# Optimization experiments

Measured on AMD Instinct MI355X. Metric: run time of the kernel, lower is better.

Reference implementation:

```python
import jax, jax.numpy as jnp
import numpy as np

NUM_HEADS = 4
HEAD_DIM = 128  # out_dim // num_heads = 512 // 4
TOP_K = 16
NEG_SLOPE = 0.2


def setup_inputs() -> dict:
    key = jax.random.key(0)
    k1, k2, k3, k4 = jax.random.split(key, 4)
    N, in_dim, out_dim = 4096, 1024, 512
    x = jax.random.normal(k1, (N, in_dim), dtype=jnp.float32)
    adj = jax.random.uniform(k2, (N, N), dtype=jnp.float32)  # all-positive, like softmax attn
    W = jax.random.normal(k3, (out_dim, in_dim), dtype=jnp.float32) * 0.02
    a = jax.random.normal(k4, (1, 2 * HEAD_DIM), dtype=jnp.float32) * 0.02
    return {"x": x, "adj": adj, "W": W, "a": a}


def reference(x, adj, W, a):
    N = x.shape[0]
    Wh = (x @ W.T).reshape(N, NUM_HEADS, HEAD_DIM)  # (N, H, D)

    # _sparsify_adj: keep top-k per row, binary mask
    k = min(TOP_K, N)
    _, topk_idx = jax.lax.top_k(adj, k)  # (N, k)
    rows = jnp.arange(N)[:, None]
    sparse = jnp.zeros_like(adj).at[rows, topk_idx].set(1.0)
    mask = sparse > 0  # (N_i, N_j)

    # a([Wh_i, Wh_j]) decomposed: a = [a_src | a_dst], score = s_i + s_j
    a_src, a_dst = a[0, :HEAD_DIM], a[0, HEAD_DIM:]
    s_i = jnp.einsum("nhd,d->nh", Wh, a_src)  # (N, H)
    s_j = jnp.einsum("nhd,d->nh", Wh, a_dst)  # (N, H)
    e = jax.nn.leaky_relu(s_i[:, None, :] + s_j[None, :, :], NEG_SLOPE)  # (N_i, N_j, H)
    e = jnp.where(mask[:, :, None], e, -jnp.inf)

    alpha = jax.nn.softmax(e, axis=1)  # softmax over neighbors j
    alpha = jnp.nan_to_num(alpha, nan=0.0)

    out = jnp.einsum("imh,mhd->ihd", alpha, Wh)  # weighted sum over j
    return jax.nn.elu(out.reshape(N, -1))  # (N, out_dim)
```

## Files before the change

### kernel.cpp

```cpp
#include <hip/hip_runtime.h>
#include <hip/hip_bf16.h>

#define N_NODES 4096
#define IN_DIM 1024
#define OUT_DIM 512
#define NUM_HEADS 4
#define HEAD_DIM 128
#define TOP_K 16
#define NEG_SLOPE 0.2f

typedef __attribute__((ext_vector_type(8))) short bf16x8;
typedef __attribute__((ext_vector_type(4))) float f32x4;

typedef __attribute__((address_space(3))) unsigned as3_u32;
typedef const __attribute__((address_space(1))) unsigned as1_u32;

static __device__ __forceinline__ void gld16(const void* g, void* l) {
    __builtin_amdgcn_global_load_lds((as1_u32*)g, (as3_u32*)l, 16, 0, 0);
}

__device__ __forceinline__ unsigned short f2bf(float f) {
    unsigned u = __float_as_uint(f);
    unsigned r = u + 0x7FFFu + ((u >> 16) & 1u);
    return (unsigned short)(r >> 16);
}
__device__ __forceinline__ float bf2f(unsigned short h) {
    return __uint_as_float(((unsigned)h) << 16);
}

__device__ __forceinline__ void conv_row(const float* __restrict__ src,
                                         unsigned short* __restrict__ dst, int t)
{
    int row = t >> 7, rem = t & 127, kb = rem >> 2, c = rem & 3;
    const float* s = src + (size_t)row * IN_DIM + kb * 32 + c * 8;
    float4 v0 = *(const float4*)s;
    float4 v1 = *(const float4*)(s + 4);
    float vv[8] = {v0.x, v0.y, v0.z, v0.w, v1.x, v1.y, v1.z, v1.w};
    bf16x8 H, L;
#pragma unroll
    for (int e = 0; e < 8; ++e) {
        unsigned short h = f2bf(vv[e]);
        H[e] = (short)h;
        L[e] = (short)f2bf(vv[e] - bf2f(h));
    }
    int sw = row & 7;
    unsigned short* base = dst + (size_t)row * 2048 + kb * 64;
    *(bf16x8*)(base + ((c ^ sw) << 3))       = H;
    *(bf16x8*)(base + (((c + 4) ^ sw) << 3)) = L;
}

#define TK_THRESH 0.988f

__device__ __forceinline__ void topk_body(int row, const float* __restrict__ adj,
                                          int* __restrict__ topkb)
{
    const int tid  = threadIdx.x;
    const int wave = tid >> 6, lane = tid & 63;
    const float* rp = adj + (size_t)row * N_NODES;

    __shared__ unsigned long long cand[4][64];
    __shared__ int wcnt[4];
    __shared__ float srow[N_NODES];

    float4 q0 = *(const float4*)(rp + wave * 1024 + 0 * 256 + lane * 4);
    float4 q1 = *(const float4*)(rp + wave * 1024 + 1 * 256 + lane * 4);
    float4 q2 = *(const float4*)(rp + wave * 1024 + 2 * 256 + lane * 4);
    float4 q3 = *(const float4*)(rp + wave * 1024 + 3 * 256 + lane * 4);

    const unsigned long long lmask = (1ull << lane) - 1ull;
    int cnt = 0;

#define FILT(qv, i, e, comp) do {                                             \
        float val = (qv).comp;                                                \
        int g = wave * 1024 + (i) * 256 + lane * 4 + (e);                     \
        bool p = val >= TK_THRESH;                                            \
        unsigned long long m = __ballot(p);                                   \
        if (p) {                                                              \
            int pos = cnt + __popcll(m & lmask);                              \
            if (pos < 64) {                                                   \
                unsigned b  = __float_as_uint(val);                           \
                unsigned mo = b ^ (unsigned)(((int)b >> 31) | 0x80000000);    \
                cand[wave][pos] =                                             \
                    ((unsigned long long)mo << 32) | (unsigned)(N_NODES - 1 - g); \
            }                                                                 \
        }                                                                     \
        cnt += __popcll(m);                                                   \
    } while (0)

    FILT(q0, 0, 0, x); FILT(q0, 0, 1, y); FILT(q0, 0, 2, z); FILT(q0, 0, 3, w);
    FILT(q1, 1, 0, x); FILT(q1, 1, 1, y); FILT(q1, 1, 2, z); FILT(q1, 1, 3, w);
    FILT(q2, 2, 0, x); FILT(q2, 2, 1, y); FILT(q2, 2, 2, z); FILT(q2, 2, 3, w);
    FILT(q3, 3, 0, x); FILT(q3, 3, 1, y); FILT(q3, 3, 2, z); FILT(q3, 3, 3, w);
#undef FILT

    if (lane == 0) wcnt[wave] = cnt;
    __syncthreads();

    const int c0n = wcnt[0], c1n = wcnt[1], c2n = wcnt[2], c3n = wcnt[3];
    const int total = c0n + c1n + c2n + c3n;
    const bool ok = (total >= TOP_K) &&
                    (c0n <= 64) && (c1n <= 64) && (c2n <= 64) && (c3n <= 64);
    int* op = topkb + (size_t)row * TOP_K;

    if (ok) {
        if (wave == 0) {
            unsigned long long k0 = lane < c0n ? cand[0][lane] : 0ull;
            unsigned long long k1 = lane < c1n ? cand[1][lane] : 0ull;
            unsigned long long k2 = lane < c2n ? cand[2][lane] : 0ull;
            unsigned long long k3 = lane < c3n ? cand[3][lane] : 0ull;
            for (int r = 0; r < TOP_K; ++r) {
                unsigned long long a01 = k0 > k1 ? k0 : k1;
                unsigned long long a23 = k2 > k3 ? k2 : k3;
                unsigned long long b = a01 > a23 ? a01 : a23;
#pragma unroll
                for (int m = 1; m < 64; m <<= 1) {
                    unsigned long long o = __shfl_xor(b, m);
                    b = o > b ? o : b;
                }
                if (lane == 0) op[r] = N_NODES - 1 - (int)(unsigned)(b & 0xFFFFFFFFu);
                if (k0 == b) k0 = 0ull;
                if (k1 == b) k1 = 0ull;
                if (k2 == b) k2 = 0ull;
                if (k3 == b) k3 = 0ull;
            }
        }
    } else {
        int base = wave * 1024 + lane * 4;
        *(float4*)&srow[base + 0 * 256] = q0;
        *(float4*)&srow[base + 1 * 256] = q1;
        *(float4*)&srow[base + 2 * 256] = q2;
        *(float4*)&srow[base + 3 * 256] = q3;
        __syncthreads();
        if (wave == 0) {
            for (int r = 0; r < TOP_K; ++r) {
                float bv = -INFINITY; int bg = 0x7fffffff;
                for (int j = 0; j < 64; ++j) {
                    int g = j * 64 + lane;
                    float val = srow[g];
                    bool better = (val > bv) || (val == bv && g < bg);
                    bv = better ? val : bv;
                    bg = better ? g : bg;
                }
#pragma unroll
                for (int m = 1; m < 64; m <<= 1) {
                    float ov = __shfl_xor(bv, m);
                    int   og = __shfl_xor(bg, m);
                    bool better = (ov > bv) || (ov == bv && og < bg);
                    bv = better ? ov : bv;
                    bg = better ? og : bg;
                }
                if (lane == 0) { op[r] = bg; srow[bg] = -INFINITY; }
            }
        }
    }
}

__global__ __launch_bounds__(256) void prep_topk_kernel(
    const float* __restrict__ x, const float* __restrict__ W,
    unsigned short* __restrict__ xc, unsigned short* __restrict__ wc,
    const float* __restrict__ adj, int* __restrict__ topkb)
{
    int b = blockIdx.x, tid = threadIdx.x;
    if (b < 4096) {
        topk_body(b, adj, topkb);
    } else if (b < 6144) {
        conv_row(x, xc, (b - 4096) * 256 + tid);
    } else {
        conv_row(W, wc, (b - 6144) * 256 + tid);
    }
}

#define GBM 64
#define GBN 64

__global__ __launch_bounds__(256, 2) void gemm_kernel(
    const unsigned short* __restrict__ xc, const unsigned short* __restrict__ wc,
    const float* __restrict__ a, unsigned short* __restrict__ Whb,
    float* __restrict__ spart)
{
    __shared__ __align__(16) unsigned short A0[GBM * 64];
    __shared__ __align__(16) unsigned short A1[GBM * 64];
    __shared__ __align__(16) unsigned short A2[GBM * 64];
    __shared__ __align__(16) unsigned short A3[GBM * 64];
    __shared__ __align__(16) unsigned short B0[GBN * 64];
    __shared__ __align__(16) unsigned short B1[GBN * 64];
    __shared__ __align__(16) unsigned short B2[GBN * 64];
    __shared__ __align__(16) unsigned short B3[GBN * 64];

    const int tid = threadIdx.x;
    const int id  = blockIdx.x;
    const int xcd = id & 7, seq = id >> 3;
    const int bm  = xcd * 8 + (seq >> 3), bn = seq & 7;

    const int wave = tid >> 6, lane = tid & 63;
    const int wm = wave >> 1, wn = wave & 1;
    const int lr = lane & 15, lk = lane >> 4;

    f32x4 acc[2][2];
#pragma unroll
    for (int i = 0; i < 2; ++i)
#pragma unroll
        for (int j = 0; j < 2; ++j) acc[i][j] = (f32x4){0.f, 0.f, 0.f, 0.f};

#define STAGE(Abuf, Bbuf, kt) do {                                            \
        size_t koff = (size_t)(kt) * 128;                                     \
        _Pragma("unroll")                                                     \
        for (int q = 0; q < 2; ++q) {               \
            int ci = q * 256 + tid;                                           \
            int row = ci >> 3, p = ci & 7;                                    \
            gld16((const char*)xc + ((size_t)(bm * GBM + row) * 4096 + koff + p * 16), \
                  (char*)(Abuf) + (size_t)ci * 16);                           \
        }                                                                     \
        _Pragma("unroll")                                                     \
        for (int q = 0; q < 2; ++q) {               \
            int ci = q * 256 + tid;                                           \
            int row = ci >> 3, p = ci & 7;                                    \
            gld16((const char*)wc + ((size_t)(bn * GBN + row) * 4096 + koff + p * 16), \
                  (char*)(Bbuf) + (size_t)ci * 16);                           \
        }                                                                     \
    } while (0)

#define COMPUTE(Abuf, Bbuf) do {                                              \
        bf16x8 bh[2], bl[2];                                                  \
        _Pragma("unroll")                                                     \
        for (int ni = 0; ni < 2; ++ni) {                                      \
            int rb = wn * 32 + ni * 16 + lr; int swb = rb & 7;                \
            bh[ni] = *(const bf16x8*)&(Bbuf)[rb * 64 + ((lk ^ swb) << 3)];    \
            bl[ni] = *(const bf16x8*)&(Bbuf)[rb * 64 + (((4 + lk) ^ swb) << 3)]; \
        }                                                                     \
        __builtin_amdgcn_s_setprio(1);                                        \
        _Pragma("unroll")                                                     \
        for (int mi = 0; mi < 2; ++mi) {                                      \
            int r = wm * 32 + mi * 16 + lr; int sw = r & 7;                   \
            bf16x8 ah = *(const bf16x8*)&(Abuf)[r * 64 + ((lk ^ sw) << 3)];   \
            bf16x8 al = *(const bf16x8*)&(Abuf)[r * 64 + (((4 + lk) ^ sw) << 3)]; \
            _Pragma("unroll")                                                 \
            for (int ni = 0; ni < 2; ++ni) {                                  \
                acc[mi][ni] = __builtin_amdgcn_mfma_f32_16x16x32_bf16(ah, bh[ni], acc[mi][ni], 0, 0, 0); \
                acc[mi][ni] = __builtin_amdgcn_mfma_f32_16x16x32_bf16(ah, bl[ni], acc[mi][ni], 0, 0, 0); \
                acc[mi][ni] = __builtin_amdgcn_mfma_f32_16x16x32_bf16(al, bh[ni], acc[mi][ni], 0, 0, 0); \
            }                                                                 \
        }                                                                     \
        __builtin_amdgcn_s_setprio(0);                                        \
    } while (0)

#define BODY(Ac, Bc, An, Bn, ktn, W) do {                                     \
        asm volatile("s_waitcnt vmcnt(" #W ")" ::: "memory");                 \
        __builtin_amdgcn_s_barrier();                                         \
        asm volatile("" ::: "memory");                                        \
        if ((ktn) < 32) STAGE(An, Bn, ktn);                                   \
        COMPUTE(Ac, Bc);                                                      \
    } while (0)

    STAGE(A0, B0, 0);
    STAGE(A1, B1, 1);
    STAGE(A2, B2, 2);

    for (int i = 0; i < 7; ++i) {
        BODY(A0, B0, A3, B3, i * 4 + 3, 8);
        BODY(A1, B1, A0, B0, i * 4 + 4, 8);
        BODY(A2, B2, A1, B1, i * 4 + 5, 8);
        BODY(A3, B3, A2, B2, i * 4 + 6, 8);
    }
    BODY(A0, B0, A3, B3, 31, 8);
    BODY(A1, B1, A0, B0, 33, 8);
    asm volatile("s_waitcnt vmcnt(4)" ::: "memory");
    __builtin_amdgcn_s_barrier();
    asm volatile("" ::: "memory");
    COMPUTE(A2, B2);
    asm volatile("s_waitcnt vmcnt(0)" ::: "memory");
    __builtin_amdgcn_s_barrier();
    asm volatile("" ::: "memory");
    COMPUTE(A3, B3);

#undef BODY
#undef COMPUTE
#undef STAGE

    const int h = bn >> 1;
    float* sps = spart + ((size_t)((bn & 1) * 2 + wn)) * 16384;
    float* spd = spart + 65536 + ((size_t)((bn & 1) * 2 + wn)) * 16384;
    float ca[2], cb[2];
#pragma unroll
    for (int ni = 0; ni < 2; ++ni) {
        int dcol = (bn & 1) * 64 + wn * 32 + ni * 16 + lr;
        ca[ni] = a[dcol];
        cb[ni] = a[HEAD_DIM + dcol];
    }
#pragma unroll
    for (int mi = 0; mi < 2; ++mi) {
        float ss[4] = {0.f, 0.f, 0.f, 0.f}, sd[4] = {0.f, 0.f, 0.f, 0.f};
#pragma unroll
        for (int ni = 0; ni < 2; ++ni) {
            int col_g = bn * GBN + wn * 32 + ni * 16 + lr;
#pragma unroll
            for (int r = 0; r < 4; ++r) {
                int row_g = bm * GBM + wm * 32 + mi * 16 + lk * 4 + r;
                float v = acc[mi][ni][r];
                Whb[(size_t)row_g * OUT_DIM + col_g] = f2bf(v);
                ss[r] += v * ca[ni];
                sd[r] += v * cb[ni];
            }
        }
#pragma unroll
        for (int s = 1; s < 16; s <<= 1)
#pragma unroll
            for (int r = 0; r < 4; ++r) {
                ss[r] += __shfl_xor(ss[r], s);
                sd[r] += __shfl_xor(sd[r], s);
            }
        if (lr == 0) {
#pragma unroll
            for (int r = 0; r < 4; ++r) {
                int row_g = bm * GBM + wm * 32 + mi * 16 + lk * 4 + r;
                sps[row_g * NUM_HEADS + h] = ss[r];
                spd[row_g * NUM_HEADS + h] = sd[r];
            }
        }
    }
}

__global__ __launch_bounds__(256) void aggregate_kernel(
    const unsigned short* __restrict__ Whb, const int* __restrict__ topk,
    const float* __restrict__ spart, float* __restrict__ out)
{
    const int i = blockIdx.x, t = threadIdx.x;
    __shared__ int   sidx[TOP_K];
    __shared__ float salpha[TOP_K][NUM_HEADS];
    __shared__ float part[3][8][64];

    if (t < 64) {
        int idxv = 0;
        if (t < TOP_K) { idxv = topk[(size_t)i * TOP_K + t]; sidx[t] = idxv; }
        int m = t >> 2, h = t & 3;
        int im = __shfl(idxv, m);
        int si = (i << 2) + h, di = (im << 2) + h;
        float e = spart[si] + spart[16384 + si] + spart[32768 + si] + spart[49152 + si]
                + spart[65536 + di] + spart[81920 + di] + spart[98304 + di] + spart[114688 + di];
        e = (e >= 0.f) ? e : NEG_SLOPE * e;
        float mx = e;
#pragma unroll
        for (int s = 4; s < 64; s <<= 1) mx = fmaxf(mx, __shfl_xor(mx, s));
        float ex = expf(e - mx);
        float sum = ex;
#pragma unroll
        for (int s = 4; s < 64; s <<= 1) sum += __shfl_xor(sum, s);
        salpha[m][h] = ex / sum;
    }
    __syncthreads();

    const int g = t >> 6, o = t & 63;
    const int h = o >> 4;
    float acc8[8] = {0.f, 0.f, 0.f, 0.f, 0.f, 0.f, 0.f, 0.f};
#pragma unroll
    for (int q = 0; q < 4; ++q) {
        int m = g * 4 + q;
        float al = salpha[m][h];
        bf16x8 v = *(const bf16x8*)&Whb[(size_t)sidx[m] * OUT_DIM + o * 8];
#pragma unroll
        for (int e = 0; e < 8; ++e)
            acc8[e] += al * bf2f((unsigned short)v[e]);
    }
    if (g) {
#pragma unroll
        for (int e = 0; e < 8; ++e) part[g - 1][e][o] = acc8[e];
    }
    __syncthreads();
    if (!g) {
        float r8[8];
#pragma unroll
        for (int e = 0; e < 8; ++e) {
            float s = acc8[e] + part[0][e][o] + part[1][e][o] + part[2][e][o];
            r8[e] = s > 0.f ? s : expf(s) - 1.f;
        }
        float4 lo = (float4){r8[0], r8[1], r8[2], r8[3]};
        float4 hi = (float4){r8[4], r8[5], r8[6], r8[7]};
        *(float4*)(out + (size_t)i * OUT_DIM + o * 8)     = lo;
        *(float4*)(out + (size_t)i * OUT_DIM + o * 8 + 4) = hi;
    }
}

extern "C" void kernel_launch(void* const* d_in, const int* in_sizes, int n_in,
                              void* d_out, int out_size, void* d_ws, size_t ws_size,
                              hipStream_t stream) {
    const float* x   = (const float*)d_in[0];
    const float* adj = (const float*)d_in[1];
    const float* W   = (const float*)d_in[2];
    const float* a   = (const float*)d_in[3];
    float* out = (float*)d_out;

    char* ws = (char*)d_ws;
    unsigned short* Whb   = (unsigned short*)ws;
    unsigned short* xc    = (unsigned short*)(ws + (8u << 20));
    unsigned short* wc    = (unsigned short*)(ws + (24u << 20));
    float*          spart = (float*)(ws + (26u << 20));
    int*            topkb = (int*)(ws + (26u << 20) + (512u << 10));

    prep_topk_kernel<<<6400, 256, 0, stream>>>(x, W, xc, wc, adj, topkb);
    gemm_kernel<<<512, 256, 0, stream>>>(xc, wc, a, Whb, spart);
    aggregate_kernel<<<N_NODES, 256, 0, stream>>>(Whb, topkb, spart, out);
}
```

Measured before the change: 142.2 us.

## Fuse top-k selection into GEMM kernel as interleaved blocks

Moves the per-row top-k selection out of the conversion kernel into the GEMM launch, interleaving one GEMM block with eight top-k blocks (4608 blocks total). The memory-bound adjacency scan can then overlap the compute-bound MFMA GEMM instead of running in the earlier serial phase. Top-k blocks reuse the GEMM's LDS buffers for candidates and fallback row storage. The trade-off is that top-k blocks now inherit the GEMM's large LDS footprint and launch bounds, which can reduce how many of them are resident at once.

Result: slower. 195.0 us (+37.2%).

```diff
diff --git a/kernel.cpp b/kernel.cpp
--- a/kernel.cpp
+++ b/kernel.cpp
@@ -49,134 +49,24 @@
     *(bf16x8*)(base + (((c + 4) ^ sw) << 3)) = L;
 }
 
-#define TK_THRESH 0.988f
-
-__device__ __forceinline__ void topk_body(int row, const float* __restrict__ adj,
-                                          int* __restrict__ topkb)
-{
-    const int tid  = threadIdx.x;
-    const int wave = tid >> 6, lane = tid & 63;
-    const float* rp = adj + (size_t)row * N_NODES;
-
-    __shared__ unsigned long long cand[4][64];
-    __shared__ int wcnt[4];
-    __shared__ float srow[N_NODES];
-
-    float4 q0 = *(const float4*)(rp + wave * 1024 + 0 * 256 + lane * 4);
-    float4 q1 = *(const float4*)(rp + wave * 1024 + 1 * 256 + lane * 4);
-    float4 q2 = *(const float4*)(rp + wave * 1024 + 2 * 256 + lane * 4);
-    float4 q3 = *(const float4*)(rp + wave * 1024 + 3 * 256 + lane * 4);
-
-    const unsigned long long lmask = (1ull << lane) - 1ull;
-    int cnt = 0;
-
-#define FILT(qv, i, e, comp) do {                                             \
-        float val = (qv).comp;                                                \
-        int g = wave * 1024 + (i) * 256 + lane * 4 + (e);                     \
-        bool p = val >= TK_THRESH;                                            \
-        unsigned long long m = __ballot(p);                                   \
-        if (p) {                                                              \
-            int pos = cnt + __popcll(m & lmask);                              \
-            if (pos < 64) {                                                   \
-                unsigned b  = __float_as_uint(val);                           \
-                unsigned mo = b ^ (unsigned)(((int)b >> 31) | 0x80000000);    \
-                cand[wave][pos] =                                             \
-                    ((unsigned long long)mo << 32) | (unsigned)(N_NODES - 1 - g); \
-            }                                                                 \
-        }                                                                     \
-        cnt += __popcll(m);                                                   \
-    } while (0)
-
-    FILT(q0, 0, 0, x); FILT(q0, 0, 1, y); FILT(q0, 0, 2, z); FILT(q0, 0, 3, w);
-    FILT(q1, 1, 0, x); FILT(q1, 1, 1, y); FILT(q1, 1, 2, z); FILT(q1, 1, 3, w);
-    FILT(q2, 2, 0, x); FILT(q2, 2, 1, y); FILT(q2, 2, 2, z); FILT(q2, 2, 3, w);
-    FILT(q3, 3, 0, x); FILT(q3, 3, 1, y); FILT(q3, 3, 2, z); FILT(q3, 3, 3, w);
-#undef FILT
-
-    if (lane == 0) wcnt[wave] = cnt;
-    __syncthreads();
-
-    const int c0n = wcnt[0], c1n = wcnt[1], c2n = wcnt[2], c3n = wcnt[3];
-    const int total = c0n + c1n + c2n + c3n;
-    const bool ok = (total >= TOP_K) &&
-                    (c0n <= 64) && (c1n <= 64) && (c2n <= 64) && (c3n <= 64);
-    int* op = topkb + (size_t)row * TOP_K;
-
-    if (ok) {
-        if (wave == 0) {
-            unsigned long long k0 = lane < c0n ? cand[0][lane] : 0ull;
-            unsigned long long k1 = lane < c1n ? cand[1][lane] : 0ull;
-            unsigned long long k2 = lane < c2n ? cand[2][lane] : 0ull;
-            unsigned long long k3 = lane < c3n ? cand[3][lane] : 0ull;
-            for (int r = 0; r < TOP_K; ++r) {
-                unsigned long long a01 = k0 > k1 ? k0 : k1;
-                unsigned long long a23 = k2 > k3 ? k2 : k3;
-                unsigned long long b = a01 > a23 ? a01 : a23;
-#pragma unroll
-                for (int m = 1; m < 64; m <<= 1) {
-                    unsigned long long o = __shfl_xor(b, m);
-                    b = o > b ? o : b;
-                }
-                if (lane == 0) op[r] = N_NODES - 1 - (int)(unsigned)(b & 0xFFFFFFFFu);
-                if (k0 == b) k0 = 0ull;
-                if (k1 == b) k1 = 0ull;
-                if (k2 == b) k2 = 0ull;
-                if (k3 == b) k3 = 0ull;
-            }
-        }
-    } else {
-        int base = wave * 1024 + lane * 4;
-        *(float4*)&srow[base + 0 * 256] = q0;
-        *(float4*)&srow[base + 1 * 256] = q1;
-        *(float4*)&srow[base + 2 * 256] = q2;
-        *(float4*)&srow[base + 3 * 256] = q3;
-        __syncthreads();
-        if (wave == 0) {
-            for (int r = 0; r < TOP_K; ++r) {
-                float bv = -INFINITY; int bg = 0x7fffffff;
-                for (int j = 0; j < 64; ++j) {
-                    int g = j * 64 + lane;
-                    float val = srow[g];
-                    bool better = (val > bv) || (val == bv && g < bg);
-                    bv = better ? val : bv;
-                    bg = better ? g : bg;
-                }
-#pragma unroll
-                for (int m = 1; m < 64; m <<= 1) {
-                    float ov = __shfl_xor(bv, m);
-                    int   og = __shfl_xor(bg, m);
-                    bool better = (ov > bv) || (ov == bv && og < bg);
-                    bv = better ? ov : bv;
-                    bg = better ? og : bg;
-                }
-                if (lane == 0) { op[r] = bg; srow[bg] = -INFINITY; }
-            }
-        }
-    }
-}
-
-__global__ __launch_bounds__(256) void prep_topk_kernel(
+__global__ __launch_bounds__(256) void prep_kernel(
     const float* __restrict__ x, const float* __restrict__ W,
-    unsigned short* __restrict__ xc, unsigned short* __restrict__ wc,
-    const float* __restrict__ adj, int* __restrict__ topkb)
+    unsigned short* __restrict__ xc, unsigned short* __restrict__ wc)
 {
     int b = blockIdx.x, tid = threadIdx.x;
-    if (b < 4096) {
-        topk_body(b, adj, topkb);
-    } else if (b < 6144) {
-        conv_row(x, xc, (b - 4096) * 256 + tid);
-    } else {
-        conv_row(W, wc, (b - 6144) * 256 + tid);
-    }
+    if (b < 2048) conv_row(x, xc, b * 256 + tid);
+    else          conv_row(W, wc, (b - 2048) * 256 + tid);
 }
 
 #define GBM 64
 #define GBN 64
-
-__global__ __launch_bounds__(256, 2) void gemm_kernel(
+#define TK_THRESH 0.988f
+
+__global__ __launch_bounds__(256, 2) void gemm_topk_kernel(
     const unsigned short* __restrict__ xc, const unsigned short* __restrict__ wc,
     const float* __restrict__ a, unsigned short* __restrict__ Whb,
-    float* __restrict__ spart)
+    float* __restrict__ spart,
+    const float* __restrict__ adj, int* __restrict__ topkb)
 {
     __shared__ __align__(16) unsigned short A0[GBM * 64];
     __shared__ __align__(16) unsigned short A1[GBM * 64];
@@ -186,33 +76,37 @@
     __shared__ __align__(16) unsigned short B1[GBN * 64];
     __shared__ __align__(16) unsigned short B2[GBN * 64];
     __shared__ __align__(16) unsigned short B3[GBN * 64];
-
+    __shared__ int wcnt4[4];
+
+    const int b   = blockIdx.x;
     const int tid = threadIdx.x;
-    const int id  = blockIdx.x;
-    const int xcd = id & 7, seq = id >> 3;
-    const int bm  = xcd * 8 + (seq >> 3), bn = seq & 7;
-
-    const int wave = tid >> 6, lane = tid & 63;
-    const int wm = wave >> 1, wn = wave & 1;
-    const int lr = lane & 15, lk = lane >> 4;
-
-    f32x4 acc[2][2];
-#pragma unroll
-    for (int i = 0; i < 2; ++i)
-#pragma unroll
-        for (int j = 0; j < 2; ++j) acc[i][j] = (f32x4){0.f, 0.f, 0.f, 0.f};
+    const int gid = b / 9;
+
+    if (b - gid * 9 == 0) {
+        const int xcd = gid & 7, seq = gid >> 3;
+        const int bm  = xcd * 8 + (seq >> 3), bn = seq & 7;
+
+        const int wave = tid >> 6, lane = tid & 63;
+        const int wm = wave >> 1, wn = wave & 1;
+        const int lr = lane & 15, lk = lane >> 4;
+
+        f32x4 acc[2][2];
+#pragma unroll
+        for (int i = 0; i < 2; ++i)
+#pragma unroll
+            for (int j = 0; j < 2; ++j) acc[i][j] = (f32x4){0.f, 0.f, 0.f, 0.f};
 
 #define STAGE(Abuf, Bbuf, kt) do {                                            \
         size_t koff = (size_t)(kt) * 128;                                     \
         _Pragma("unroll")                                                     \
-        for (int q = 0; q < 2; ++q) {               \
+        for (int q = 0; q < 2; ++q) {                                         \
             int ci = q * 256 + tid;                                           \
             int row = ci >> 3, p = ci & 7;                                    \
             gld16((const char*)xc + ((size_t)(bm * GBM + row) * 4096 + koff + p * 16), \
                   (char*)(Abuf) + (size_t)ci * 16);                           \
         }                                                                     \
         _Pragma("unroll")                                                     \
-        for (int q = 0; q < 2; ++q) {               \
+        for (int q = 0; q < 2; ++q) {                                         \
             int ci = q * 256 + tid;                                           \
             int row = ci >> 3, p = ci & 7;                                    \
             gld16((const char*)wc + ((size_t)(bn * GBN + row) * 4096 + koff + p * 16), \
@@ -252,69 +146,174 @@
         COMPUTE(Ac, Bc);                                                      \
     } while (0)
 
-    STAGE(A0, B0, 0);
-    STAGE(A1, B1, 1);
-    STAGE(A2, B2, 2);
-
-    for (int i = 0; i < 7; ++i) {
-        BODY(A0, B0, A3, B3, i * 4 + 3, 8);
-        BODY(A1, B1, A0, B0, i * 4 + 4, 8);
-        BODY(A2, B2, A1, B1, i * 4 + 5, 8);
-        BODY(A3, B3, A2, B2, i * 4 + 6, 8);
-    }
-    BODY(A0, B0, A3, B3, 31, 8);
-    BODY(A1, B1, A0, B0, 33, 8);
-    asm volatile("s_waitcnt vmcnt(4)" ::: "memory");
-    __builtin_amdgcn_s_barrier();
-    asm volatile("" ::: "memory");
-    COMPUTE(A2, B2);
-    asm volatile("s_waitcnt vmcnt(0)" ::: "memory");
-    __builtin_amdgcn_s_barrier();
-    asm volatile("" ::: "memory");
-    COMPUTE(A3, B3);
+        STAGE(A0, B0, 0);
+        STAGE(A1, B1, 1);
+        STAGE(A2, B2, 2);
+
+        for (int i = 0; i < 7; ++i) {
+            BODY(A0, B0, A3, B3, i * 4 + 3, 8);
+            BODY(A1, B1, A0, B0, i * 4 + 4, 8);
+            BODY(A2, B2, A1, B1, i * 4 + 5, 8);
+            BODY(A3, B3, A2, B2, i * 4 + 6, 8);
+        }
+        BODY(A0, B0, A3, B3, 31, 8);
+        BODY(A1, B1, A0, B0, 33, 8);
+        asm volatile("s_waitcnt vmcnt(4)" ::: "memory");
+        __builtin_amdgcn_s_barrier();
+        asm volatile("" ::: "memory");
+        COMPUTE(A2, B2);
+        asm volatile("s_waitcnt vmcnt(0)" ::: "memory");
+        __builtin_amdgcn_s_barrier();
+        asm volatile("" ::: "memory");
+        COMPUTE(A3, B3);
 
 #undef BODY
 #undef COMPUTE
 #undef STAGE
 
-    const int h = bn >> 1;
-    float* sps = spart + ((size_t)((bn & 1) * 2 + wn)) * 16384;
-    float* spd = spart + 65536 + ((size_t)((bn & 1) * 2 + wn)) * 16384;
-    float ca[2], cb[2];
-#pragma unroll
-    for (int ni = 0; ni < 2; ++ni) {
-        int dcol = (bn & 1) * 64 + wn * 32 + ni * 16 + lr;
-        ca[ni] = a[dcol];
-        cb[ni] = a[HEAD_DIM + dcol];
-    }
-#pragma unroll
-    for (int mi = 0; mi < 2; ++mi) {
-        float ss[4] = {0.f, 0.f, 0.f, 0.f}, sd[4] = {0.f, 0.f, 0.f, 0.f};
+        const int h = bn >> 1;
+        float* sps = spart + ((size_t)((bn & 1) * 2 + wn)) * 16384;
+        float* spd = spart + 65536 + ((size_t)((bn & 1) * 2 + wn)) * 16384;
+        float ca[2], cb[2];
 #pragma unroll
         for (int ni = 0; ni < 2; ++ni) {
-            int col_g = bn * GBN + wn * 32 + ni * 16 + lr;
-#pragma unroll
-            for (int r = 0; r < 4; ++r) {
-                int row_g = bm * GBM + wm * 32 + mi * 16 + lk * 4 + r;
-                float v = acc[mi][ni][r];
-                Whb[(size_t)row_g * OUT_DIM + col_g] = f2bf(v);
-                ss[r] += v * ca[ni];
-                sd[r] += v * cb[ni];
+            int dcol = (bn & 1) * 64 + wn * 32 + ni * 16 + lr;
+            ca[ni] = a[dcol];
+            cb[ni] = a[HEAD_DIM + dcol];
+        }
+#pragma unroll
+        for (int mi = 0; mi < 2; ++mi) {
+            float ss[4] = {0.f, 0.f, 0.f, 0.f}, sd[4] = {0.f, 0.f, 0.f, 0.f};
+#pragma unroll
+            for (int ni = 0; ni < 2; ++ni) {
+                int col_g = bn * GBN + wn * 32 + ni * 16 + lr;
+#pragma unroll
+                for (int r = 0; r < 4; ++r) {
+                    int row_g = bm * GBM + wm * 32 + mi * 16 + lk * 4 + r;
+                    float v = acc[mi][ni][r];
+                    Whb[(size_t)row_g * OUT_DIM + col_g] = f2bf(v);
+                    ss[r] += v * ca[ni];
+                    sd[r] += v * cb[ni];
+                }
+            }
+#pragma unroll
+            for (int s = 1; s < 16; s <<= 1)
+#pragma unroll
+                for (int r = 0; r < 4; ++r) {
+                    ss[r] += __shfl_xor(ss[r], s);
+                    sd[r] += __shfl_xor(sd[r], s);
+                }
+            if (lr == 0) {
+#pragma unroll
+                for (int r = 0; r < 4; ++r) {
+                    int row_g = bm * GBM + wm * 32 + mi * 16 + lk * 4 + r;
+                    sps[row_g * NUM_HEADS + h] = ss[r];
+                    spd[row_g * NUM_HEADS + h] = sd[r];
+                }
             }
         }
-#pragma unroll
-        for (int s = 1; s < 16; s <<= 1)
-#pragma unroll
-            for (int r = 0; r < 4; ++r) {
-                ss[r] += __shfl_xor(ss[r], s);
-                sd[r] += __shfl_xor(sd[r], s);
+    } else {
+        const int row = b - gid - 1;
+        const int wave = tid >> 6, lane = tid & 63;
+        const float* rp = adj + (size_t)row * N_NODES;
+
+        unsigned long long* cand = (unsigned long long*)B0;
+        float* sr0 = (float*)A0;
+        float* sr1 = (float*)A1;
+
+        float4 q0 = *(const float4*)(rp + wave * 1024 + 0 * 256 + lane * 4);
+        float4 q1 = *(const float4*)(rp + wave * 1024 + 1 * 256 + lane * 4);
+        float4 q2 = *(const float4*)(rp + wave * 1024 + 2 * 256 + lane * 4);
+        float4 q3 = *(const float4*)(rp + wave * 1024 + 3 * 256 + lane * 4);
+
+        const unsigned long long lmask = (1ull << lane) - 1ull;
+        int cnt = 0;
+
+#define FILT(qv, i, e, comp) do {                                             \
+        float val = (qv).comp;                                                \
+        int g = wave * 1024 + (i) * 256 + lane * 4 + (e);                     \
+        bool p = val >= TK_THRESH;                                            \
+        unsigned long long m = __ballot(p);                                   \
+        if (p) {                                                              \
+            int pos = cnt + __popcll(m & lmask);                              \
+            if (pos < 64) {                                                   \
+                unsigned bb = __float_as_uint(val);                           \
+                unsigned mo = bb ^ (unsigned)(((int)bb >> 31) | 0x80000000);  \
+                cand[wave * 64 + pos] =                                       \
+                    ((unsigned long long)mo << 32) | (unsigned)(N_NODES - 1 - g); \
+            }                                                                 \
+        }                                                                     \
+        cnt += __popcll(m);                                                   \
+    } while (0)
+
+        FILT(q0, 0, 0, x); FILT(q0, 0, 1, y); FILT(q0, 0, 2, z); FILT(q0, 0, 3, w);
+        FILT(q1, 1, 0, x); FILT(q1, 1, 1, y); FILT(q1, 1, 2, z); FILT(q1, 1, 3, w);
+        FILT(q2, 2, 0, x); FILT(q2, 2, 1, y); FILT(q2, 2, 2, z); FILT(q2, 2, 3, w);
+        FILT(q3, 3, 0, x); FILT(q3, 3, 1, y); FILT(q3, 3, 2, z); FILT(q3, 3, 3, w);
+#undef FILT
+
+        if (lane == 0) wcnt4[wave] = cnt;
+        __syncthreads();
+
+        const int c0n = wcnt4[0], c1n = wcnt4[1], c2n = wcnt4[2], c3n = wcnt4[3];
+        const int total = c0n + c1n + c2n + c3n;
+        const bool ok = (total >= TOP_K) &&
+                        (c0n <= 64) && (c1n <= 64) && (c2n <= 64) && (c3n <= 64);
+        int* op = topkb + (size_t)row * TOP_K;
+
+        if (ok) {
+            if (wave == 0) {
+                unsigned long long k0 = lane < c0n ? cand[0 * 64 + lane] : 0ull;
+                unsigned long long k1 = lane < c1n ? cand[1 * 64 + lane] : 0ull;
+                unsigned long long k2 = lane < c2n ? cand[2 * 64 + lane] : 0ull;
+                unsigned long long k3 = lane < c3n ? cand[3 * 64 + lane] : 0ull;
+                for (int r = 0; r < TOP_K; ++r) {
+                    unsigned long long a01 = k0 > k1 ? k0 : k1;
+                    unsigned long long a23 = k2 > k3 ? k2 : k3;
+                    unsigned long long bb = a01 > a23 ? a01 : a23;
+#pragma unroll
+                    for (int m = 1; m < 64; m <<= 1) {
+                        unsigned long long o = __shfl_xor(bb, m);
+                        bb = o > bb ? o : bb;
+                    }
+                    if (lane == 0) op[r] = N_NODES - 1 - (int)(unsigned)(bb & 0xFFFFFFFFu);
+                    if (k0 == bb) k0 = 0ull;
+                    if (k1 == bb) k1 = 0ull;
+                    if (k2 == bb) k2 = 0ull;
+                    if (k3 == bb) k3 = 0ull;
+                }
             }
-        if (lr == 0) {
-#pragma unroll
-            for (int r = 0; r < 4; ++r) {
-                int row_g = bm * GBM + wm * 32 + mi * 16 + lk * 4 + r;
-                sps[row_g * NUM_HEADS + h] = ss[r];
-                spd[row_g * NUM_HEADS + h] = sd[r];
+        } else {
+            int base = wave * 1024 + lane * 4;
+            float* dst = (wave < 2) ? sr0 + base : sr1 + (base - 2048);
+            *(float4*)(dst + 0 * 256) = q0;
+            *(float4*)(dst + 1 * 256) = q1;
+            *(float4*)(dst + 2 * 256) = q2;
+            *(float4*)(dst + 3 * 256) = q3;
+            __syncthreads();
+            if (wave == 0) {
+                for (int r = 0; r < TOP_K; ++r) {
+                    float bv = -INFINITY; int bg = 0x7fffffff;
+                    for (int j = 0; j < 64; ++j) {
+                        int g = j * 64 + lane;
+                        float val = g < 2048 ? sr0[g] : sr1[g - 2048];
+                        bool better = (val > bv) || (val == bv && g < bg);
+                        bv = better ? val : bv;
+                        bg = better ? g : bg;
+                    }
+#pragma unroll
+                    for (int m = 1; m < 64; m <<= 1) {
+                        float ov = __shfl_xor(bv, m);
+                        int   og = __shfl_xor(bg, m);
+                        bool better = (ov > bv) || (ov == bv && og < bg);
+                        bv = better ? ov : bv;
+                        bg = better ? og : bg;
+                    }
+                    if (lane == 0) {
+                        op[r] = bg;
+                        if (bg < 2048) sr0[bg] = -INFINITY; else sr1[bg - 2048] = -INFINITY;
+                    }
+                }
             }
         }
     }
@@ -396,7 +395,7 @@
     float*          spart = (float*)(ws + (26u << 20));
     int*            topkb = (int*)(ws + (26u << 20) + (512u << 10));
 
-    prep_topk_kernel<<<6400, 256, 0, stream>>>(x, W, xc, wc, adj, topkb);
-    gemm_kernel<<<512, 256, 0, stream>>>(xc, wc, a, Whb, spart);
+    prep_kernel<<<2304, 256, 0, stream>>>(x, W, xc, wc);
+    gemm_topk_kernel<<<4608, 256, 0, stream>>>(xc, wc, a, Whb, spart, adj, topkb);
     aggregate_kernel<<<N_NODES, 256, 0, stream>>>(Whb, topkb, spart, out);
 }
```
